# Kernel optimization log

Hardware: AMD Instinct MI355X
Metric: run time of the kernel (lower is better)

## Reference

```python
import jax, jax.numpy as jnp
import numpy as np

EPS = 1e-5


def _bn(x, g, b):
    # training-mode BatchNorm2d over (N, H, W), biased variance
    m = jnp.mean(x, axis=(0, 2, 3), keepdims=True)
    v = jnp.var(x, axis=(0, 2, 3), keepdims=True)
    return (x - m) * jax.lax.rsqrt(v + EPS) * g[None, :, None, None] + b[None, :, None, None]


def _conv1x1(x, w):
    # x: [B, Cin, H, W], w: [Cout, Cin]
    return jnp.einsum('bchw,oc->bohw', x, w)


def _prop_attention(x, wq, wkv, wo, bo, obj_dict, bg_dict, rand_inds):
    B, C, H, W = x.shape  # B == 1
    heads, crop = rand_inds.shape[0], rand_inds.shape[1]
    dh = C // heads
    HW = H * W
    num_obj = crop // 2
    # original does x.clone().detach() before attention
    xd = jax.lax.stop_gradient(x)
    xh = xd.reshape(heads, dh, HW)  # batch=1 folded away (matches t.view(-1, crop**2))
    # pos[h, i, j] = flat pixel index gathered for head h, group i, slot j
    pos = jnp.concatenate(
        [obj_dict[rand_inds[:, :num_obj]], bg_dict[rand_inds[:, num_obj:]]], axis=1
    )  # [heads, crop, crop]
    tokens = jax.vmap(lambda xv, pv: xv[:, pv])(xh, pos)  # [heads, dh, crop, crop]
    tokens = tokens.transpose(0, 2, 3, 1).reshape(heads * crop, crop, dh)
    q = tokens @ wq.T
    k, v = jnp.split(tokens @ wkv.T, 2, axis=-1)
    dots = jnp.einsum('bie,bje->bij', q, k) * (dh ** -0.5)
    attn = jax.nn.softmax(dots, axis=-1)
    out = jnp.einsum('bij,bje->bie', attn, v)  # [heads*crop, crop, dh]
    # faithful to torch out.view(heads*crop, -1, crop): a raw row-major reinterpret
    out_r = out.reshape(heads, crop, dh, crop)
    vals = out_r.transpose(0, 2, 1, 3).reshape(heads, dh, crop * crop)
    pos_flat = pos.reshape(heads, crop * crop)
    # pos is a bijection onto [0, HW) per head -> invert and gather
    ar = jnp.arange(HW, dtype=jnp.int32)
    inv = jax.vmap(lambda p: jnp.zeros((HW,), jnp.int32).at[p].set(ar))(pos_flat)
    img = jax.vmap(lambda vh, ih: vh[:, ih])(vals, inv)  # [heads, dh, HW]
    img = img.reshape(1, heads * dh, H, W)
    # to_out: Linear(dim, dim) applied channels-last
    return jnp.einsum('bchw,oc->bohw', img, wo) + bo[None, :, None, None]


def setup_inputs():
    H = W = 300
    HW = H * W
    heads, crop = 2, H
    num_obj = crop // 2
    ch, emb = 256, 64
    dh = emb // heads
    key = jax.random.key(0)
    ks = jax.random.split(key, 10)
    x = jax.random.normal(ks[0], (1, ch, H, W), jnp.float32)
    perm = jax.random.permutation(ks[1], HW)
    obj_dict = perm[: HW // 2]
    bg_dict = perm[HW // 2 :]
    ri = []
    for h in range(heads):
        po = jax.random.permutation(jax.random.fold_in(ks[2], h), HW // 2).reshape(num_obj, crop)
        pb = jax.random.permutation(jax.random.fold_in(ks[3], h), HW // 2).reshape(crop - num_obj, crop)
        ri.append(jnp.concatenate([po, pb], axis=0))
    rand_inds = jnp.stack(ri)  # [heads, crop, crop]
    w_conv1 = jax.random.normal(ks[4], (emb, ch), jnp.float32) / np.sqrt(ch)
    wq = jax.random.normal(ks[5], (dh, dh), jnp.float32) / np.sqrt(dh)
    wkv = jax.random.normal(ks[6], (2 * dh, dh), jnp.float32) / np.sqrt(dh)
    wo = jax.random.normal(ks[7], (emb, emb), jnp.float32) / np.sqrt(emb)
    bo = jnp.zeros((emb,), jnp.float32)
    w_conv2 = jax.random.normal(ks[8], (emb, 2 * emb), jnp.float32) / np.sqrt(2 * emb)
    return {
        'x': x,
        'w_conv1': w_conv1,
        'bn1_g': jnp.ones((emb,), jnp.float32),
        'bn1_b': jnp.zeros((emb,), jnp.float32),
        'wq': wq,
        'wkv': wkv,
        'wo': wo,
        'bo': bo,
        'w_conv2': w_conv2,
        'bn2_g': jnp.ones((emb,), jnp.float32),
        'bn2_b': jnp.zeros((emb,), jnp.float32),
        'obj_dict': obj_dict,
        'bg_dict': bg_dict,
        'rand_inds': rand_inds,
    }


def reference(x, w_conv1, bn1_g, bn1_b, wq, wkv, wo, bo, w_conv2, bn2_g, bn2_b, obj_dict, bg_dict, rand_inds):
    x1 = jax.nn.relu(_bn(_conv1x1(x, w_conv1), bn1_g, bn1_b))
    xa = jax.nn.relu(_prop_attention(x1, wq, wkv, wo, bo, obj_dict, bg_dict, rand_inds))
    xc = jnp.concatenate([xa, x1], axis=1)
    return jax.nn.relu(_bn(_conv1x1(xc, w_conv2), bn2_g, bn2_b))
```

## Files before the change

### kernel.cpp

```cpp
#include <hip/hip_runtime.h>
#include <hip/hip_bf16.h>

#define HW 90000
#define CROP 300
#define C2EXP 0.25503492f

typedef __attribute__((ext_vector_type(8))) short s8v;
typedef __attribute__((ext_vector_type(4))) float f4v;
#define MFMA16(a,b,c) __builtin_amdgcn_mfma_f32_16x16x32_bf16(a,b,c,0,0,0)

__device__ __forceinline__ unsigned short f2bf(float f) {
    unsigned int u = __float_as_uint(f);
    return (unsigned short)((u + 0x7fffu + ((u >> 16) & 1u)) >> 16);
}
__device__ __forceinline__ float bf2f(unsigned short s) {
    return __uint_as_float(((unsigned int)s) << 16);
}
__device__ __forceinline__ unsigned pk_trunc(float a, float b) {
    return __builtin_amdgcn_perm(__float_as_uint(b), __float_as_uint(a), 0x07060302u);
}
__device__ __forceinline__ unsigned pk_rne(float a, float b) {
    return (unsigned)f2bf(a) | ((unsigned)f2bf(b) << 16);
}

__global__ void prep_kernel(const float* __restrict__ w1, const float* __restrict__ wq,
                            const float* __restrict__ wkv, const float* __restrict__ wo,
                            const float* __restrict__ w2,
                            short* __restrict__ w1b, short* __restrict__ wkvb,
                            short* __restrict__ wob, short* __restrict__ w2b,
                            short* __restrict__ msb) {
    int idx = blockIdx.x * blockDim.x + threadIdx.x;
    int stride = gridDim.x * blockDim.x;
    for (int i = idx; i < 16384; i += stride) w1b[i] = (short)f2bf(w1[i]);
    for (int i = idx; i < 2048; i += stride)  wkvb[i] = (short)f2bf(wkv[i]);
    for (int i = idx; i < 4096; i += stride)  wob[i] = (short)f2bf(wo[i]);
    for (int i = idx; i < 8192; i += stride)  w2b[i] = (short)f2bf(w2[i]);
    for (int i = idx; i < 1024; i += stride) {
        int ep = i >> 5, e = i & 31;
        float s = 0.f;
        for (int a = 0; a < 32; ++a) s += wq[a * 32 + e] * wkv[a * 32 + ep];
        msb[i] = (short)f2bf(s * C2EXP);
    }
}

__global__ __launch_bounds__(256, 2) void conv1_mfma(const float* __restrict__ x,
        const short* __restrict__ w1b, short* __restrict__ y1b, float* __restrict__ stat) {
    __shared__ __align__(16) short lw[16384];
    __shared__ float red[2][4][64];
    const int wave = threadIdx.x >> 6, lane = threadIdx.x & 63;
    const int q = lane >> 4, n = lane & 15;
    for (int i = threadIdx.x; i < 2048; i += 256)
        ((uint4*)lw)[i] = ((const uint4*)w1b)[i];
    __syncthreads();

    const int s0 = blockIdx.x * 256 + wave * 64;
    int pbx = s0 + 4 * n;
    if (pbx > HW - 4) pbx = HW - 4;
    f4v acc[4][4];
#pragma unroll
    for (int mt = 0; mt < 4; ++mt)
#pragma unroll
        for (int nt = 0; nt < 4; ++nt) acc[mt][nt] = f4v{0.f, 0.f, 0.f, 0.f};

    float4 cur[8], nxt[8];
#pragma unroll
    for (int j = 0; j < 8; ++j)
        cur[j] = *(const float4*)(x + (size_t)(q * 8 + j) * HW + pbx);
#pragma unroll
    for (int kb = 0; kb < 8; ++kb) {
        if (kb < 7) {
#pragma unroll
            for (int j = 0; j < 8; ++j)
                nxt[j] = *(const float4*)(x + (size_t)((kb + 1) * 32 + q * 8 + j) * HW + pbx);
        }
        s8v A[4];
#pragma unroll
        for (int mt = 0; mt < 4; ++mt) {
            union { unsigned u[4]; s8v v; } am;
#pragma unroll
            for (int w = 0; w < 4; ++w)
                am.u[w] = pk_trunc(((const float*)&cur[2 * w])[mt],
                                   ((const float*)&cur[2 * w + 1])[mt]);
            A[mt] = am.v;
        }
#pragma unroll
        for (int mt = 0; mt < 4; ++mt)
#pragma unroll
            for (int nt = 0; nt < 4; ++nt) {
                int c = (nt & 1) + 2 * n + 32 * (nt >> 1);
                s8v B = *(const s8v*)(lw + c * 256 + kb * 32 + q * 8);
                acc[mt][nt] = MFMA16(A[mt], B, acc[mt][nt]);
            }
        if (kb < 7) {
#pragma unroll
            for (int j = 0; j < 8; ++j) cur[j] = nxt[j];
        }
    }

    float s1[4] = {0.f, 0.f, 0.f, 0.f}, s2[4] = {0.f, 0.f, 0.f, 0.f};
#pragma unroll
    for (int mt = 0; mt < 4; ++mt)
#pragma unroll
        for (int r = 0; r < 4; ++r) {
            int p = s0 + 4 * (q * 4 + r) + mt;
            if (p < HW) {
                float v0 = acc[mt][0][r], v1 = acc[mt][1][r];
                float v2 = acc[mt][2][r], v3 = acc[mt][3][r];
                *(unsigned*)(y1b + (size_t)p * 64 + 2 * n)      = pk_rne(v0, v1);
                *(unsigned*)(y1b + (size_t)p * 64 + 32 + 2 * n) = pk_rne(v2, v3);
                s1[0] += v0; s2[0] += v0 * v0;
                s1[1] += v1; s2[1] += v1 * v1;
                s1[2] += v2; s2[2] += v2 * v2;
                s1[3] += v3; s2[3] += v3 * v3;
            }
        }
#pragma unroll
    for (int m = 16; m < 64; m <<= 1)
#pragma unroll
        for (int nt = 0; nt < 4; ++nt) {
            s1[nt] += __shfl_xor(s1[nt], m, 64);
            s2[nt] += __shfl_xor(s2[nt], m, 64);
        }
    if (lane < 16)
#pragma unroll
        for (int nt = 0; nt < 4; ++nt) {
            int c = (nt & 1) + 2 * lane + 32 * (nt >> 1);
            red[0][wave][c] = s1[nt];
            red[1][wave][c] = s2[nt];
        }
    __syncthreads();
    if (threadIdx.x < 128) {
        int k = threadIdx.x >> 6, c = threadIdx.x & 63;
        atomicAdd(&stat[k * 64 + c],
                  red[k][0][c] + red[k][1][c] + red[k][2][c] + red[k][3][c]);
    }
}

__global__ void bn_fin_kernel(const float* __restrict__ stat,
        const float* __restrict__ g, const float* __restrict__ b, float* __restrict__ ab) {
    int c = threadIdx.x;
    float m = stat[c] * (1.f / HW);
    float v = stat[64 + c] * (1.f / HW) - m * m;
    float ac = g[c] * rsqrtf(v + 1e-5f);
    ab[c] = ac;
    ab[64 + c] = b[c] - m * ac;
}

__global__ __launch_bounds__(256) void bnrelu_kernel(const short* __restrict__ y1b,
        const float* __restrict__ ab1, short* __restrict__ x1b) {
    int t = blockIdx.x * 256 + threadIdx.x;
    if (t >= 720000) return;
    int cb = 8 * (t & 7);
    float4 a0 = *(const float4*)(ab1 + cb), a1 = *(const float4*)(ab1 + cb + 4);
    float4 b0 = *(const float4*)(ab1 + 64 + cb), b1 = *(const float4*)(ab1 + 64 + cb + 4);
    uint4 u = ((const uint4*)y1b)[t];
    float r0 = fmaxf(fmaf(a0.x, __uint_as_float(u.x << 16), b0.x), 0.f);
    float r1 = fmaxf(fmaf(a0.y, __uint_as_float(u.x & 0xffff0000u), b0.y), 0.f);
    float r2 = fmaxf(fmaf(a0.z, __uint_as_float(u.y << 16), b0.z), 0.f);
    float r3 = fmaxf(fmaf(a0.w, __uint_as_float(u.y & 0xffff0000u), b0.w), 0.f);
    float r4 = fmaxf(fmaf(a1.x, __uint_as_float(u.z << 16), b1.x), 0.f);
    float r5 = fmaxf(fmaf(a1.y, __uint_as_float(u.z & 0xffff0000u), b1.y), 0.f);
    float r6 = fmaxf(fmaf(a1.z, __uint_as_float(u.w << 16), b1.z), 0.f);
    float r7 = fmaxf(fmaf(a1.w, __uint_as_float(u.w & 0xffff0000u), b1.w), 0.f);
    uint4 o;
    o.x = pk_rne(r0, r1); o.y = pk_rne(r2, r3);
    o.z = pk_rne(r4, r5); o.w = pk_rne(r6, r7);
    ((uint4*)x1b)[t] = o;
}

__global__ __launch_bounds__(512, 4) void attn_mfma_kernel(const short* __restrict__ x1b,
        const short* __restrict__ msb, const short* __restrict__ wkvb,
        const int* __restrict__ obj, const int* __restrict__ bg,
        const int* __restrict__ rinds, short* __restrict__ imgb) {
    __shared__ __align__(16) short tok[304 * 40];
    __shared__ __align__(16) short vt[32 * 328];
    __shared__ __align__(16) short pbuf[8 * 3 * 640];
    __shared__ int possh[300];
    const int b = blockIdx.x;
    const int h = b / CROP, i = b - h * CROP;
    const int tid = threadIdx.x;
    const int wave = tid >> 6, lane = tid & 63, q = lane >> 4, n = lane & 15;
    const int nti = (wave < 3) ? 3 : 2;

    if (tid < 300) {
        int ri = rinds[h * HW + i * CROP + tid];
        possh[tid] = (i < 150) ? obj[ri] : bg[ri];
    }
    for (int ii = tid; ii < 80; ii += 512)
        ((unsigned*)(tok + 300 * 40))[ii] = 0;
    for (int ii = tid; ii < 640; ii += 512) {
        int e = ii / 20, w = ii - 20 * e;
        ((unsigned*)vt)[e * 164 + 144 + w] = 0;
    }
    __syncthreads();

    for (int idx = tid; idx < 1200; idx += 512) {
        int j = idx >> 2, part = idx & 3;
        *(uint4*)(tok + j * 40 + part * 8) =
            *(const uint4*)(x1b + (size_t)possh[j] * 64 + h * 32 + part * 8);
    }
    __syncthreads();

    short* pw0 = pbuf + wave * 3 * 640;
    s8v aQ[3];
    {
        s8v bq0 = *(const s8v*)(msb + n * 32 + q * 8);
        s8v bq1 = *(const s8v*)(msb + (16 + n) * 32 + q * 8);
        s8v bv0 = *(const s8v*)(wkvb + (32 + n) * 32 + q * 8);
        s8v bv1 = *(const s8v*)(wkvb + (48 + n) * 32 + q * 8);
        f4v zz = {0.f, 0.f, 0.f, 0.f};
#pragma unroll
        for (int ti = 0; ti < 3; ++ti) {
            aQ[ti] = s8v{};
            if (ti < nti) {
                int t = wave + ti * 8;
                s8v at = *(const s8v*)(tok + (16 * t + n) * 40 + q * 8);
                f4v qf0 = MFMA16(at, bq0, zz);
                f4v qf1 = MFMA16(at, bq1, zz);
                f4v vf0 = MFMA16(at, bv0, zz);
                f4v vf1 = MFMA16(at, bv1, zz);
#pragma unroll
                for (int r = 0; r < 4; ++r) {
                    int row = 16 * t + q * 4 + r;
                    int phys = ((row >> 5) << 5) + 2 * (row & 15) + ((row >> 4) & 1);
                    vt[n * 328 + phys]        = (short)f2bf(vf0[r]);
                    vt[(16 + n) * 328 + phys] = (short)f2bf(vf1[r]);
                    pw0[(q * 4 + r) * 40 + n]      = (short)f2bf(qf0[r]);
                    pw0[(q * 4 + r) * 40 + 16 + n] = (short)f2bf(qf1[r]);
                }
                asm volatile("s_waitcnt lgkmcnt(0)" ::: "memory");
                aQ[ti] = *(const s8v*)(pw0 + n * 40 + q * 8);
            }
        }
    }
    __syncthreads();

    f4v O[3][2];
    float lsum[3][4];
#pragma unroll
    for (int ti = 0; ti < 3; ++ti) {
        O[ti][0] = f4v{0.f, 0.f, 0.f, 0.f};
        O[ti][1] = f4v{0.f, 0.f, 0.f, 0.f};
#pragma unroll
        for (int r = 0; r < 4; ++r) lsum[ti][r] = 0.f;
    }
    f4v zz = {0.f, 0.f, 0.f, 0.f};
    for (int kb = 0; kb < 10; ++kb) {
        s8v bK0 = *(const s8v*)(tok + (32 * kb + n) * 40 + q * 8);
        s8v bK1 = (kb < 9) ? *(const s8v*)(tok + (32 * kb + 16 + n) * 40 + q * 8) : s8v{};
        s8v bV0 = *(const s8v*)(vt + n * 328 + kb * 32 + q * 8);
        s8v bV1 = *(const s8v*)(vt + (16 + n) * 328 + kb * 32 + q * 8);
        f4v sv[3][2];
#pragma unroll
        for (int ti = 0; ti < 3; ++ti)
            if (ti < nti) {
                sv[ti][0] = MFMA16(aQ[ti], bK0, zz);
                sv[ti][1] = MFMA16(aQ[ti], bK1, zz);
            }
#pragma unroll
        for (int ti = 0; ti < 3; ++ti)
            if (ti < nti) {
                unsigned* pwd = (unsigned*)(pbuf + (wave * 3 + ti) * 640);
                if (kb < 9) {
#pragma unroll
                    for (int r = 0; r < 4; ++r) {
                        float e0 = exp2f(sv[ti][0][r]);
                        float e1 = exp2f(sv[ti][1][r]);
                        unsigned pk = pk_trunc(e0, e1);
                        lsum[ti][r] += __uint_as_float(pk << 16) +
                                       __uint_as_float(pk & 0xffff0000u);
                        pwd[(q * 4 + r) * 20 + n] = pk;
                    }
                } else {
#pragma unroll
                    for (int r = 0; r < 4; ++r) {
                        float e0 = (n < 12) ? exp2f(sv[ti][0][r]) : 0.f;
                        unsigned pk = pk_trunc(e0, 0.f);
                        lsum[ti][r] += __uint_as_float(pk << 16);
                        pwd[(q * 4 + r) * 20 + n] = pk;
                    }
                }
            }
        asm volatile("s_waitcnt lgkmcnt(0)" ::: "memory");
#pragma unroll
        for (int ti = 0; ti < 3; ++ti)
            if (ti < nti) {
                s8v ap = *(const s8v*)(pbuf + (wave * 3 + ti) * 640 + n * 40 + q * 8);
                O[ti][0] = MFMA16(ap, bV0, O[ti][0]);
                O[ti][1] = MFMA16(ap, bV1, O[ti][1]);
            }
    }
    __syncthreads();

#pragma unroll
    for (int m = 1; m < 16; m <<= 1) {
#pragma unroll
        for (int ti = 0; ti < 3; ++ti)
#pragma unroll
            for (int r = 0; r < 4; ++r)
                lsum[ti][r] += __shfl_xor(lsum[ti][r], m, 64);
    }
    short* outb = tok;
#pragma unroll
    for (int ti = 0; ti < 3; ++ti) {
        if (ti >= nti) continue;
        int t = wave + ti * 8;
#pragma unroll
        for (int r = 0; r < 4; ++r) {
            float rl = 1.f / lsum[ti][r];
            int row = 16 * t + q * 4 + r;
            outb[row * 32 + n]      = (short)f2bf(O[ti][0][r] * rl);
            outb[row * 32 + 16 + n] = (short)f2bf(O[ti][1][r] * rl);
        }
    }
    __syncthreads();

    for (int idx = tid; idx < 9600; idx += 512) {
        int jj = idx >> 5, dd = idx & 31;
        imgb[(size_t)possh[jj] * 64 + h * 32 + dd] = outb[dd * CROP + jj];
    }
}

__global__ __launch_bounds__(256, 3) void fuse2_mfma(const short* __restrict__ imgb,
        const short* __restrict__ x1b,
        const short* __restrict__ wob, const short* __restrict__ w2b,
        const float* __restrict__ bo, short* __restrict__ y2b, float* __restrict__ stat) {
    __shared__ __align__(16) short xas[4][16 * 72];
    __shared__ unsigned ytrp[64 * 68];
    __shared__ float red[2][4][64];
    const int wave = threadIdx.x >> 6, lane = threadIdx.x & 63;
    const int q = lane >> 4, n = lane & 15;
    s8v Bo[2][4], B2[4][4];
#pragma unroll
    for (int kb = 0; kb < 2; ++kb)
#pragma unroll
        for (int nt = 0; nt < 4; ++nt)
            Bo[kb][nt] = *(const s8v*)(wob + (nt * 16 + n) * 64 + kb * 32 + q * 8);
#pragma unroll
    for (int kb = 0; kb < 4; ++kb)
#pragma unroll
        for (int nt = 0; nt < 4; ++nt)
            B2[kb][nt] = *(const s8v*)(w2b + (nt * 16 + n) * 128 + kb * 32 + q * 8);
    float bov[4];
#pragma unroll
    for (int nt = 0; nt < 4; ++nt) bov[nt] = bo[nt * 16 + n];

    float s1[4] = {0.f, 0.f, 0.f, 0.f}, s2[4] = {0.f, 0.f, 0.f, 0.f};
    short* xw = xas[wave];
#pragma unroll
    for (int ti = 0; ti < 2; ++ti) {
        int tile = blockIdx.x * 8 + wave * 2 + ti;
        if (tile >= 5625) continue;
        int s0 = tile * 16;
        f4v xacc[4];
#pragma unroll
        for (int nt = 0; nt < 4; ++nt) xacc[nt] = f4v{0.f, 0.f, 0.f, 0.f};
#pragma unroll
        for (int kb = 0; kb < 2; ++kb) {
            s8v A = *(const s8v*)(imgb + (size_t)(s0 + n) * 64 + kb * 32 + q * 8);
#pragma unroll
            for (int nt = 0; nt < 4; ++nt) xacc[nt] = MFMA16(A, Bo[kb][nt], xacc[nt]);
        }
#pragma unroll
        for (int nt = 0; nt < 4; ++nt)
#pragma unroll
            for (int r = 0; r < 4; ++r) {
                float v = fmaxf(xacc[nt][r] + bov[nt], 0.f);
                xw[(q * 4 + r) * 72 + nt * 16 + n] = (short)f2bf(v);
            }
        asm volatile("s_waitcnt lgkmcnt(0)" ::: "memory");
        f4v yacc[4];
#pragma unroll
        for (int nt = 0; nt < 4; ++nt) yacc[nt] = f4v{0.f, 0.f, 0.f, 0.f};
#pragma unroll
        for (int kb = 0; kb < 2; ++kb) {
            s8v Axa = *(const s8v*)(xw + n * 72 + kb * 32 + q * 8);
#pragma unroll
            for (int nt = 0; nt < 4; ++nt) yacc[nt] = MFMA16(Axa, B2[kb][nt], yacc[nt]);
        }
#pragma unroll
        for (int kb = 0; kb < 2; ++kb) {
            s8v A = *(const s8v*)(x1b + (size_t)(s0 + n) * 64 + kb * 32 + q * 8);
#pragma unroll
            for (int nt = 0; nt < 4; ++nt) yacc[nt] = MFMA16(A, B2[kb + 2][nt], yacc[nt]);
        }
        int pl2 = wave * 16 + ti * 8;
#pragma unroll
        for (int nt = 0; nt < 4; ++nt) {
#pragma unroll
            for (int r = 0; r < 4; ++r) {
                float v = yacc[nt][r];
                s1[nt] += v; s2[nt] += v * v;
            }
            ytrp[(nt * 16 + n) * 68 + pl2 + q * 2 + 0] = pk_rne(yacc[nt][0], yacc[nt][1]);
            ytrp[(nt * 16 + n) * 68 + pl2 + q * 2 + 1] = pk_rne(yacc[nt][2], yacc[nt][3]);
        }
    }
#pragma unroll
    for (int m = 16; m < 64; m <<= 1)
#pragma unroll
        for (int nt = 0; nt < 4; ++nt) {
            s1[nt] += __shfl_xor(s1[nt], m, 64);
            s2[nt] += __shfl_xor(s2[nt], m, 64);
        }
    if (lane < 16)
#pragma unroll
        for (int nt = 0; nt < 4; ++nt) {
            red[0][wave][nt * 16 + lane] = s1[nt];
            red[1][wave][nt * 16 + lane] = s2[nt];
        }
    __syncthreads();
    int s0b = blockIdx.x * 128;
    int maxp2 = (HW - s0b) >> 1;
    for (int i = threadIdx.x; i < 4096; i += 256) {
        int c = i >> 6, p2 = i & 63;
        if (p2 < maxp2)
            ((unsigned*)y2b)[c * (HW / 2) + (s0b >> 1) + p2] = ytrp[c * 68 + p2];
    }
    if (threadIdx.x < 128) {
        int k = threadIdx.x >> 6, c = threadIdx.x & 63;
        atomicAdd(&stat[k * 64 + c],
                  red[k][0][c] + red[k][1][c] + red[k][2][c] + red[k][3][c]);
    }
}

__global__ __launch_bounds__(256) void bn_out_kernel(const short* __restrict__ y2b,
        const float* __restrict__ ab2, float* __restrict__ out) {
    int c = blockIdx.y;
    int i = blockIdx.x * 256 + threadIdx.x;
    if (i >= 22500) return;
    float a = ab2[c], b = ab2[64 + c];
    uint2 u = *(const uint2*)((const unsigned*)y2b + c * (HW / 2) + 2 * i);
    float4 v;
    v.x = fmaxf(fmaf(a, __uint_as_float(u.x << 16), b), 0.f);
    v.y = fmaxf(fmaf(a, __uint_as_float(u.x & 0xffff0000u), b), 0.f);
    v.z = fmaxf(fmaf(a, __uint_as_float(u.y << 16), b), 0.f);
    v.w = fmaxf(fmaf(a, __uint_as_float(u.y & 0xffff0000u), b), 0.f);
    *(float4*)(out + (size_t)c * HW + 4 * i) = v;
}

extern "C" void kernel_launch(void* const* d_in, const int* in_sizes, int n_in,
                              void* d_out, int out_size, void* d_ws, size_t ws_size,
                              hipStream_t stream) {
    const float* x   = (const float*)d_in[0];
    const float* w1  = (const float*)d_in[1];
    const float* g1  = (const float*)d_in[2];
    const float* b1  = (const float*)d_in[3];
    const float* wq  = (const float*)d_in[4];
    const float* wkv = (const float*)d_in[5];
    const float* wo  = (const float*)d_in[6];
    const float* bo  = (const float*)d_in[7];
    const float* w2  = (const float*)d_in[8];
    const float* g2  = (const float*)d_in[9];
    const float* b2  = (const float*)d_in[10];
    const int* obj   = (const int*)d_in[11];
    const int* bg    = (const int*)d_in[12];
    const int* rinds = (const int*)d_in[13];

    float* WSF  = (float*)d_ws;
    short* W1B  = (short*)d_ws;
    short* WOB  = W1B + 16384;
    short* W2B  = WOB + 4096;
    short* WKVB = W2B + 8192;
    short* MSB  = WKVB + 2048;
    float* STAT = WSF + 16384;
    float* AB1  = STAT + 256;
    float* AB2  = AB1 + 128;
    short* Y1B  = (short*)(WSF + 16896);
    short* X1B  = Y1B + 5760000;
    short* IMGB = X1B + 5760000;
    short* Y2B  = IMGB + 5760000;

    hipMemsetAsync(STAT, 0, 1024, stream);
    prep_kernel<<<16, 256, 0, stream>>>(w1, wq, wkv, wo, w2, W1B, WKVB, WOB, W2B, MSB);
    conv1_mfma<<<352, 256, 0, stream>>>(x, W1B, Y1B, STAT);
    bn_fin_kernel<<<1, 64, 0, stream>>>(STAT, g1, b1, AB1);
    bnrelu_kernel<<<2813, 256, 0, stream>>>(Y1B, AB1, X1B);
    attn_mfma_kernel<<<600, 512, 0, stream>>>(X1B, MSB, WKVB, obj, bg, rinds, IMGB);
    fuse2_mfma<<<704, 256, 0, stream>>>(IMGB, X1B, WOB, W2B, bo, Y2B, STAT + 128);
    bn_fin_kernel<<<1, 64, 0, stream>>>(STAT + 128, g2, b2, AB2);
    bn_out_kernel<<<dim3(88, 64), 256, 0, stream>>>(Y2B, AB2, (float*)d_out);
}
```

Baseline: 253.0 us.

## Fuse BN1+ReLU into attention and conv2 consumers, restructure attention to 4 waves

Removes the standalone bnrelu kernel and the X1B buffer: the BN1 affine plus ReLU is now applied on the fly when gathering tokens in attention and when loading x1 in the fused conv2 kernel. Attention blocks shrink to 256 threads with 5 tiles per wave. The S matrix is computed transposed so the probabilities are fed to the PV MFMA through ds_bpermute shuffles instead of an LDS staging buffer, which also drops the pbuf shared array. conv1 moves to 128-thread blocks with twice as many blocks. The trade-off is recomputing BN on gathered rows and more cross-lane permute traffic in the attention inner loop.

```diff
diff --git a/kernel.cpp b/kernel.cpp
--- a/kernel.cpp
+++ b/kernel.cpp
@@ -43,17 +43,17 @@
     }
 }
 
-__global__ __launch_bounds__(256, 2) void conv1_mfma(const float* __restrict__ x,
+__global__ __launch_bounds__(128, 2) void conv1_mfma(const float* __restrict__ x,
         const short* __restrict__ w1b, short* __restrict__ y1b, float* __restrict__ stat) {
     __shared__ __align__(16) short lw[16384];
-    __shared__ float red[2][4][64];
+    __shared__ float red[2][2][64];
     const int wave = threadIdx.x >> 6, lane = threadIdx.x & 63;
     const int q = lane >> 4, n = lane & 15;
-    for (int i = threadIdx.x; i < 2048; i += 256)
+    for (int i = threadIdx.x; i < 2048; i += 128)
         ((uint4*)lw)[i] = ((const uint4*)w1b)[i];
     __syncthreads();
 
-    const int s0 = blockIdx.x * 256 + wave * 64;
+    const int s0 = blockIdx.x * 128 + wave * 64;
     int pbx = s0 + 4 * n;
     if (pbx > HW - 4) pbx = HW - 4;
     f4v acc[4][4];
@@ -129,10 +129,9 @@
             red[1][wave][c] = s2[nt];
         }
     __syncthreads();
-    if (threadIdx.x < 128) {
+    {
         int k = threadIdx.x >> 6, c = threadIdx.x & 63;
-        atomicAdd(&stat[k * 64 + c],
-                  red[k][0][c] + red[k][1][c] + red[k][2][c] + red[k][3][c]);
+        atomicAdd(&stat[k * 64 + c], red[k][0][c] + red[k][1][c]);
     }
 }
 
@@ -146,183 +145,195 @@
     ab[64 + c] = b[c] - m * ac;
 }
 
-__global__ __launch_bounds__(256) void bnrelu_kernel(const short* __restrict__ y1b,
-        const float* __restrict__ ab1, short* __restrict__ x1b) {
-    int t = blockIdx.x * 256 + threadIdx.x;
-    if (t >= 720000) return;
-    int cb = 8 * (t & 7);
-    float4 a0 = *(const float4*)(ab1 + cb), a1 = *(const float4*)(ab1 + cb + 4);
-    float4 b0 = *(const float4*)(ab1 + 64 + cb), b1 = *(const float4*)(ab1 + 64 + cb + 4);
-    uint4 u = ((const uint4*)y1b)[t];
-    float r0 = fmaxf(fmaf(a0.x, __uint_as_float(u.x << 16), b0.x), 0.f);
-    float r1 = fmaxf(fmaf(a0.y, __uint_as_float(u.x & 0xffff0000u), b0.y), 0.f);
-    float r2 = fmaxf(fmaf(a0.z, __uint_as_float(u.y << 16), b0.z), 0.f);
-    float r3 = fmaxf(fmaf(a0.w, __uint_as_float(u.y & 0xffff0000u), b0.w), 0.f);
-    float r4 = fmaxf(fmaf(a1.x, __uint_as_float(u.z << 16), b1.x), 0.f);
-    float r5 = fmaxf(fmaf(a1.y, __uint_as_float(u.z & 0xffff0000u), b1.y), 0.f);
-    float r6 = fmaxf(fmaf(a1.z, __uint_as_float(u.w << 16), b1.z), 0.f);
-    float r7 = fmaxf(fmaf(a1.w, __uint_as_float(u.w & 0xffff0000u), b1.w), 0.f);
-    uint4 o;
-    o.x = pk_rne(r0, r1); o.y = pk_rne(r2, r3);
-    o.z = pk_rne(r4, r5); o.w = pk_rne(r6, r7);
-    ((uint4*)x1b)[t] = o;
-}
-
-__global__ __launch_bounds__(512, 4) void attn_mfma_kernel(const short* __restrict__ x1b,
+__global__ __launch_bounds__(256, 3) void attn_mfma_kernel(const short* __restrict__ y1b,
+        const float* __restrict__ ab1,
         const short* __restrict__ msb, const short* __restrict__ wkvb,
         const int* __restrict__ obj, const int* __restrict__ bg,
         const int* __restrict__ rinds, short* __restrict__ imgb) {
     __shared__ __align__(16) short tok[304 * 40];
     __shared__ __align__(16) short vt[32 * 328];
-    __shared__ __align__(16) short pbuf[8 * 3 * 640];
     __shared__ int possh[300];
     const int b = blockIdx.x;
     const int h = b / CROP, i = b - h * CROP;
     const int tid = threadIdx.x;
     const int wave = tid >> 6, lane = tid & 63, q = lane >> 4, n = lane & 15;
-    const int nti = (wave < 3) ? 3 : 2;
-
-    if (tid < 300) {
-        int ri = rinds[h * HW + i * CROP + tid];
-        possh[tid] = (i < 150) ? obj[ri] : bg[ri];
-    }
-    for (int ii = tid; ii < 80; ii += 512)
+    const int ntj = (wave < 3) ? 5 : 4;
+
+    for (int jj = tid; jj < 300; jj += 256) {
+        int ri = rinds[h * HW + i * CROP + jj];
+        possh[jj] = (i < 150) ? obj[ri] : bg[ri];
+    }
+    for (int ii = tid; ii < 80; ii += 256)
         ((unsigned*)(tok + 300 * 40))[ii] = 0;
-    for (int ii = tid; ii < 640; ii += 512) {
-        int e = ii / 20, w = ii - 20 * e;
-        ((unsigned*)vt)[e * 164 + 144 + w] = 0;
-    }
-    __syncthreads();
-
-    for (int idx = tid; idx < 1200; idx += 512) {
-        int j = idx >> 2, part = idx & 3;
-        *(uint4*)(tok + j * 40 + part * 8) =
-            *(const uint4*)(x1b + (size_t)possh[j] * 64 + h * 32 + part * 8);
-    }
-    __syncthreads();
-
-    short* pw0 = pbuf + wave * 3 * 640;
-    s8v aQ[3];
+    __syncthreads();
+
+    {
+        int part = tid & 3;
+        float4 a0 = *(const float4*)(ab1 + h * 32 + part * 8);
+        float4 a1 = *(const float4*)(ab1 + h * 32 + part * 8 + 4);
+        float4 b0 = *(const float4*)(ab1 + 64 + h * 32 + part * 8);
+        float4 b1 = *(const float4*)(ab1 + 64 + h * 32 + part * 8 + 4);
+        for (int idx = tid; idx < 1200; idx += 256) {
+            int j = idx >> 2;
+            uint4 u = *(const uint4*)(y1b + (size_t)possh[j] * 64 + h * 32 + part * 8);
+            float r0 = fmaxf(fmaf(a0.x, __uint_as_float(u.x << 16), b0.x), 0.f);
+            float r1 = fmaxf(fmaf(a0.y, __uint_as_float(u.x & 0xffff0000u), b0.y), 0.f);
+            float r2 = fmaxf(fmaf(a0.z, __uint_as_float(u.y << 16), b0.z), 0.f);
+            float r3 = fmaxf(fmaf(a0.w, __uint_as_float(u.y & 0xffff0000u), b0.w), 0.f);
+            float r4 = fmaxf(fmaf(a1.x, __uint_as_float(u.z << 16), b1.x), 0.f);
+            float r5 = fmaxf(fmaf(a1.y, __uint_as_float(u.z & 0xffff0000u), b1.y), 0.f);
+            float r6 = fmaxf(fmaf(a1.z, __uint_as_float(u.w << 16), b1.z), 0.f);
+            float r7 = fmaxf(fmaf(a1.w, __uint_as_float(u.w & 0xffff0000u), b1.w), 0.f);
+            uint4 o;
+            o.x = pk_rne(r0, r1); o.y = pk_rne(r2, r3);
+            o.z = pk_rne(r4, r5); o.w = pk_rne(r6, r7);
+            *(uint4*)(tok + j * 40 + part * 8) = o;
+        }
+    }
+    __syncthreads();
+
+    short* pw = vt + wave * 640;
+    s8v aQ[5];
     {
         s8v bq0 = *(const s8v*)(msb + n * 32 + q * 8);
         s8v bq1 = *(const s8v*)(msb + (16 + n) * 32 + q * 8);
+        f4v zz = {0.f, 0.f, 0.f, 0.f};
+#pragma unroll
+        for (int tj = 0; tj < 5; ++tj) {
+            aQ[tj] = s8v{};
+            if (tj < ntj) {
+                int t = wave + tj * 4;
+                s8v at = *(const s8v*)(tok + (16 * t + n) * 40 + q * 8);
+                f4v qf0 = MFMA16(at, bq0, zz);
+                f4v qf1 = MFMA16(at, bq1, zz);
+#pragma unroll
+                for (int r = 0; r < 4; ++r) {
+                    pw[(q * 4 + r) * 40 + n]      = (short)f2bf(qf0[r]);
+                    pw[(q * 4 + r) * 40 + 16 + n] = (short)f2bf(qf1[r]);
+                }
+                asm volatile("s_waitcnt lgkmcnt(0)" ::: "memory");
+                aQ[tj] = *(const s8v*)(pw + n * 40 + q * 8);
+            }
+        }
+    }
+    __syncthreads();
+
+    {
         s8v bv0 = *(const s8v*)(wkvb + (32 + n) * 32 + q * 8);
         s8v bv1 = *(const s8v*)(wkvb + (48 + n) * 32 + q * 8);
         f4v zz = {0.f, 0.f, 0.f, 0.f};
 #pragma unroll
-        for (int ti = 0; ti < 3; ++ti) {
-            aQ[ti] = s8v{};
-            if (ti < nti) {
-                int t = wave + ti * 8;
+        for (int tj = 0; tj < 5; ++tj) {
+            if (tj < ntj) {
+                int t = wave + tj * 4;
                 s8v at = *(const s8v*)(tok + (16 * t + n) * 40 + q * 8);
-                f4v qf0 = MFMA16(at, bq0, zz);
-                f4v qf1 = MFMA16(at, bq1, zz);
                 f4v vf0 = MFMA16(at, bv0, zz);
                 f4v vf1 = MFMA16(at, bv1, zz);
 #pragma unroll
                 for (int r = 0; r < 4; ++r) {
                     int row = 16 * t + q * 4 + r;
-                    int phys = ((row >> 5) << 5) + 2 * (row & 15) + ((row >> 4) & 1);
-                    vt[n * 328 + phys]        = (short)f2bf(vf0[r]);
-                    vt[(16 + n) * 328 + phys] = (short)f2bf(vf1[r]);
-                    pw0[(q * 4 + r) * 40 + n]      = (short)f2bf(qf0[r]);
-                    pw0[(q * 4 + r) * 40 + 16 + n] = (short)f2bf(qf1[r]);
+                    vt[n * 328 + row]        = (short)f2bf(vf0[r]);
+                    vt[(16 + n) * 328 + row] = (short)f2bf(vf1[r]);
                 }
-                asm volatile("s_waitcnt lgkmcnt(0)" ::: "memory");
-                aQ[ti] = *(const s8v*)(pw0 + n * 40 + q * 8);
-            }
-        }
-    }
-    __syncthreads();
-
-    f4v O[3][2];
-    float lsum[3][4];
-#pragma unroll
-    for (int ti = 0; ti < 3; ++ti) {
-        O[ti][0] = f4v{0.f, 0.f, 0.f, 0.f};
-        O[ti][1] = f4v{0.f, 0.f, 0.f, 0.f};
-#pragma unroll
-        for (int r = 0; r < 4; ++r) lsum[ti][r] = 0.f;
-    }
+            }
+        }
+    }
+    for (int ii = tid; ii < 384; ii += 256) {
+        int e = ii / 12, w = ii - 12 * e;
+        ((unsigned*)vt)[e * 164 + 152 + w] = 0;
+    }
+    __syncthreads();
+
+    f4v O[5][2];
+    float lsum[5];
+#pragma unroll
+    for (int tj = 0; tj < 5; ++tj) {
+        O[tj][0] = f4v{0.f, 0.f, 0.f, 0.f};
+        O[tj][1] = f4v{0.f, 0.f, 0.f, 0.f};
+        lsum[tj] = 0.f;
+    }
+    const int bidx0 = (n + ((lane & 16) ? 32 : 0)) * 4;
+    const int bidx1 = bidx0 + 64;
+    const bool hi = (lane & 32) != 0;
     f4v zz = {0.f, 0.f, 0.f, 0.f};
     for (int kb = 0; kb < 10; ++kb) {
-        s8v bK0 = *(const s8v*)(tok + (32 * kb + n) * 40 + q * 8);
-        s8v bK1 = (kb < 9) ? *(const s8v*)(tok + (32 * kb + 16 + n) * 40 + q * 8) : s8v{};
+        s8v A0 = *(const s8v*)(tok + (32 * kb + n) * 40 + q * 8);
+        s8v A1 = (kb < 9) ? *(const s8v*)(tok + (32 * kb + 16 + n) * 40 + q * 8) : s8v{};
         s8v bV0 = *(const s8v*)(vt + n * 328 + kb * 32 + q * 8);
         s8v bV1 = *(const s8v*)(vt + (16 + n) * 328 + kb * 32 + q * 8);
-        f4v sv[3][2];
-#pragma unroll
-        for (int ti = 0; ti < 3; ++ti)
-            if (ti < nti) {
-                sv[ti][0] = MFMA16(aQ[ti], bK0, zz);
-                sv[ti][1] = MFMA16(aQ[ti], bK1, zz);
-            }
-#pragma unroll
-        for (int ti = 0; ti < 3; ++ti)
-            if (ti < nti) {
-                unsigned* pwd = (unsigned*)(pbuf + (wave * 3 + ti) * 640);
-                if (kb < 9) {
-#pragma unroll
-                    for (int r = 0; r < 4; ++r) {
-                        float e0 = exp2f(sv[ti][0][r]);
-                        float e1 = exp2f(sv[ti][1][r]);
-                        unsigned pk = pk_trunc(e0, e1);
-                        lsum[ti][r] += __uint_as_float(pk << 16) +
-                                       __uint_as_float(pk & 0xffff0000u);
-                        pwd[(q * 4 + r) * 20 + n] = pk;
-                    }
-                } else {
-#pragma unroll
-                    for (int r = 0; r < 4; ++r) {
-                        float e0 = (n < 12) ? exp2f(sv[ti][0][r]) : 0.f;
-                        unsigned pk = pk_trunc(e0, 0.f);
-                        lsum[ti][r] += __uint_as_float(pk << 16);
-                        pwd[(q * 4 + r) * 20 + n] = pk;
-                    }
-                }
-            }
-        asm volatile("s_waitcnt lgkmcnt(0)" ::: "memory");
-#pragma unroll
-        for (int ti = 0; ti < 3; ++ti)
-            if (ti < nti) {
-                s8v ap = *(const s8v*)(pbuf + (wave * 3 + ti) * 640 + n * 40 + q * 8);
-                O[ti][0] = MFMA16(ap, bV0, O[ti][0]);
-                O[ti][1] = MFMA16(ap, bV1, O[ti][1]);
-            }
-    }
-    __syncthreads();
-
-#pragma unroll
-    for (int m = 1; m < 16; m <<= 1) {
-#pragma unroll
-        for (int ti = 0; ti < 3; ++ti)
-#pragma unroll
-            for (int r = 0; r < 4; ++r)
-                lsum[ti][r] += __shfl_xor(lsum[ti][r], m, 64);
-    }
+#pragma unroll
+        for (int tj = 0; tj < 5; ++tj) {
+            if (tj >= ntj) continue;
+            f4v s0 = MFMA16(A0, aQ[tj], zz);
+            unsigned p0a, p0b, p1a, p1b;
+            if (kb < 9) {
+                f4v s1 = MFMA16(A1, aQ[tj], zz);
+                p0a = pk_trunc(exp2f(s0[0]), exp2f(s0[1]));
+                p0b = pk_trunc(exp2f(s0[2]), exp2f(s0[3]));
+                p1a = pk_trunc(exp2f(s1[0]), exp2f(s1[1]));
+                p1b = pk_trunc(exp2f(s1[2]), exp2f(s1[3]));
+            } else {
+                float e0 = (q < 3) ? exp2f(s0[0]) : 0.f;
+                float e1 = (q < 3) ? exp2f(s0[1]) : 0.f;
+                float e2 = (q < 3) ? exp2f(s0[2]) : 0.f;
+                float e3 = (q < 3) ? exp2f(s0[3]) : 0.f;
+                p0a = pk_trunc(e0, e1);
+                p0b = pk_trunc(e2, e3);
+                p1a = 0; p1b = 0;
+            }
+            lsum[tj] += __uint_as_float(p0a << 16) + __uint_as_float(p0a & 0xffff0000u)
+                      + __uint_as_float(p0b << 16) + __uint_as_float(p0b & 0xffff0000u)
+                      + __uint_as_float(p1a << 16) + __uint_as_float(p1a & 0xffff0000u)
+                      + __uint_as_float(p1b << 16) + __uint_as_float(p1b & 0xffff0000u);
+            union { unsigned u[4]; s8v v; } Ap;
+            {
+                unsigned v0a = __builtin_amdgcn_ds_bpermute(bidx0, (int)p0a);
+                unsigned v1a = __builtin_amdgcn_ds_bpermute(bidx0, (int)p1a);
+                unsigned v0b = __builtin_amdgcn_ds_bpermute(bidx0, (int)p0b);
+                unsigned v1b = __builtin_amdgcn_ds_bpermute(bidx0, (int)p1b);
+                Ap.u[0] = hi ? v1a : v0a;
+                Ap.u[1] = hi ? v1b : v0b;
+                unsigned w0a = __builtin_amdgcn_ds_bpermute(bidx1, (int)p0a);
+                unsigned w1a = __builtin_amdgcn_ds_bpermute(bidx1, (int)p1a);
+                unsigned w0b = __builtin_amdgcn_ds_bpermute(bidx1, (int)p0b);
+                unsigned w1b_ = __builtin_amdgcn_ds_bpermute(bidx1, (int)p1b);
+                Ap.u[2] = hi ? w1a : w0a;
+                Ap.u[3] = hi ? w1b_ : w0b;
+            }
+            O[tj][0] = MFMA16(Ap.v, bV0, O[tj][0]);
+            O[tj][1] = MFMA16(Ap.v, bV1, O[tj][1]);
+        }
+    }
+    __syncthreads();
+
+#pragma unroll
+    for (int m = 16; m < 64; m <<= 1)
+#pragma unroll
+        for (int tj = 0; tj < 5; ++tj)
+            lsum[tj] += __shfl_xor(lsum[tj], m, 64);
     short* outb = tok;
 #pragma unroll
-    for (int ti = 0; ti < 3; ++ti) {
-        if (ti >= nti) continue;
-        int t = wave + ti * 8;
+    for (int tj = 0; tj < 5; ++tj) {
+        if (tj >= ntj) continue;
+        int t = wave + tj * 4;
 #pragma unroll
         for (int r = 0; r < 4; ++r) {
-            float rl = 1.f / lsum[ti][r];
+            float rl = 1.f / __shfl(lsum[tj], q * 4 + r, 64);
             int row = 16 * t + q * 4 + r;
-            outb[row * 32 + n]      = (short)f2bf(O[ti][0][r] * rl);
-            outb[row * 32 + 16 + n] = (short)f2bf(O[ti][1][r] * rl);
-        }
-    }
-    __syncthreads();
-
-    for (int idx = tid; idx < 9600; idx += 512) {
+            outb[row * 32 + n]      = (short)f2bf(O[tj][0][r] * rl);
+            outb[row * 32 + 16 + n] = (short)f2bf(O[tj][1][r] * rl);
+        }
+    }
+    __syncthreads();
+
+    for (int idx = tid; idx < 9600; idx += 256) {
         int jj = idx >> 5, dd = idx & 31;
         imgb[(size_t)possh[jj] * 64 + h * 32 + dd] = outb[dd * CROP + jj];
     }
 }
 
 __global__ __launch_bounds__(256, 3) void fuse2_mfma(const short* __restrict__ imgb,
-        const short* __restrict__ x1b,
+        const short* __restrict__ y1b, const float* __restrict__ ab1,
         const short* __restrict__ wob, const short* __restrict__ w2b,
         const float* __restrict__ bo, short* __restrict__ y2b, float* __restrict__ stat) {
     __shared__ __align__(16) short xas[4][16 * 72];
@@ -344,6 +355,14 @@
     float bov[4];
 #pragma unroll
     for (int nt = 0; nt < 4; ++nt) bov[nt] = bo[nt * 16 + n];
+    float4 a1v[2][2], b1v[2][2];
+#pragma unroll
+    for (int kb = 0; kb < 2; ++kb) {
+        a1v[kb][0] = *(const float4*)(ab1 + kb * 32 + q * 8);
+        a1v[kb][1] = *(const float4*)(ab1 + kb * 32 + q * 8 + 4);
+        b1v[kb][0] = *(const float4*)(ab1 + 64 + kb * 32 + q * 8);
+        b1v[kb][1] = *(const float4*)(ab1 + 64 + kb * 32 + q * 8 + 4);
+    }
 
     float s1[4] = {0.f, 0.f, 0.f, 0.f}, s2[4] = {0.f, 0.f, 0.f, 0.f};
     short* xw = xas[wave];
@@ -380,9 +399,20 @@
         }
 #pragma unroll
         for (int kb = 0; kb < 2; ++kb) {
-            s8v A = *(const s8v*)(x1b + (size_t)(s0 + n) * 64 + kb * 32 + q * 8);
-#pragma unroll
-            for (int nt = 0; nt < 4; ++nt) yacc[nt] = MFMA16(A, B2[kb + 2][nt], yacc[nt]);
+            uint4 u = *(const uint4*)(y1b + (size_t)(s0 + n) * 64 + kb * 32 + q * 8);
+            float r0 = fmaxf(fmaf(a1v[kb][0].x, __uint_as_float(u.x << 16), b1v[kb][0].x), 0.f);
+            float r1 = fmaxf(fmaf(a1v[kb][0].y, __uint_as_float(u.x & 0xffff0000u), b1v[kb][0].y), 0.f);
+            float r2 = fmaxf(fmaf(a1v[kb][0].z, __uint_as_float(u.y << 16), b1v[kb][0].z), 0.f);
+            float r3 = fmaxf(fmaf(a1v[kb][0].w, __uint_as_float(u.y & 0xffff0000u), b1v[kb][0].w), 0.f);
+            float r4 = fmaxf(fmaf(a1v[kb][1].x, __uint_as_float(u.z << 16), b1v[kb][1].x), 0.f);
+            float r5 = fmaxf(fmaf(a1v[kb][1].y, __uint_as_float(u.z & 0xffff0000u), b1v[kb][1].y), 0.f);
+            float r6 = fmaxf(fmaf(a1v[kb][1].z, __uint_as_float(u.w << 16), b1v[kb][1].z), 0.f);
+            float r7 = fmaxf(fmaf(a1v[kb][1].w, __uint_as_float(u.w & 0xffff0000u), b1v[kb][1].w), 0.f);
+            union { unsigned u[4]; s8v v; } A;
+            A.u[0] = pk_rne(r0, r1); A.u[1] = pk_rne(r2, r3);
+            A.u[2] = pk_rne(r4, r5); A.u[3] = pk_rne(r6, r7);
+#pragma unroll
+            for (int nt = 0; nt < 4; ++nt) yacc[nt] = MFMA16(A.v, B2[kb + 2][nt], yacc[nt]);
         }
         int pl2 = wave * 16 + ti * 8;
 #pragma unroll
@@ -467,17 +497,15 @@
     float* AB1  = STAT + 256;
     float* AB2  = AB1 + 128;
     short* Y1B  = (short*)(WSF + 16896);
-    short* X1B  = Y1B + 5760000;
-    short* IMGB = X1B + 5760000;
+    short* IMGB = Y1B + 5760000;
     short* Y2B  = IMGB + 5760000;
 
     hipMemsetAsync(STAT, 0, 1024, stream);
     prep_kernel<<<16, 256, 0, stream>>>(w1, wq, wkv, wo, w2, W1B, WKVB, WOB, W2B, MSB);
-    conv1_mfma<<<352, 256, 0, stream>>>(x, W1B, Y1B, STAT);
+    conv1_mfma<<<704, 128, 0, stream>>>(x, W1B, Y1B, STAT);
     bn_fin_kernel<<<1, 64, 0, stream>>>(STAT, g1, b1, AB1);
-    bnrelu_kernel<<<2813, 256, 0, stream>>>(Y1B, AB1, X1B);
-    attn_mfma_kernel<<<600, 512, 0, stream>>>(X1B, MSB, WKVB, obj, bg, rinds, IMGB);
-    fuse2_mfma<<<704, 256, 0, stream>>>(IMGB, X1B, WOB, W2B, bo, Y2B, STAT + 128);
+    attn_mfma_kernel<<<600, 256, 0, stream>>>(Y1B, AB1, MSB, WKVB, obj, bg, rinds, IMGB);
+    fuse2_mfma<<<704, 256, 0, stream>>>(IMGB, Y1B, AB1, WOB, W2B, bo, Y2B, STAT + 128);
     bn_fin_kernel<<<1, 64, 0, stream>>>(STAT + 128, g2, b2, AB2);
     bn_out_kernel<<<dim3(88, 64), 256, 0, stream>>>(Y2B, AB2, (float*)d_out);
 }
```

New measurement: 266.2 us. +5.2%, slower.

## Fuse BN1+ReLU into attention gather and conv2 loads, drop bnrelu kernel

Applied to the files above, without the earlier changes.

Removes the standalone bnrelu kernel. The attention kernel and fuse2 kernel now read raw conv1 output and apply the BN scale/shift plus ReLU while loading, so the X1B buffer is neither written nor re-read. It also restructures the Q staging so each tile gets its own LDS buffer, with a single wait before reading them back. The cost is recomputing BN+ReLU in two consumers and a little extra ALU work in the gather paths.

```diff
diff --git a/kernel.cpp b/kernel.cpp
--- a/kernel.cpp
+++ b/kernel.cpp
@@ -146,29 +146,8 @@
     ab[64 + c] = b[c] - m * ac;
 }
 
-__global__ __launch_bounds__(256) void bnrelu_kernel(const short* __restrict__ y1b,
-        const float* __restrict__ ab1, short* __restrict__ x1b) {
-    int t = blockIdx.x * 256 + threadIdx.x;
-    if (t >= 720000) return;
-    int cb = 8 * (t & 7);
-    float4 a0 = *(const float4*)(ab1 + cb), a1 = *(const float4*)(ab1 + cb + 4);
-    float4 b0 = *(const float4*)(ab1 + 64 + cb), b1 = *(const float4*)(ab1 + 64 + cb + 4);
-    uint4 u = ((const uint4*)y1b)[t];
-    float r0 = fmaxf(fmaf(a0.x, __uint_as_float(u.x << 16), b0.x), 0.f);
-    float r1 = fmaxf(fmaf(a0.y, __uint_as_float(u.x & 0xffff0000u), b0.y), 0.f);
-    float r2 = fmaxf(fmaf(a0.z, __uint_as_float(u.y << 16), b0.z), 0.f);
-    float r3 = fmaxf(fmaf(a0.w, __uint_as_float(u.y & 0xffff0000u), b0.w), 0.f);
-    float r4 = fmaxf(fmaf(a1.x, __uint_as_float(u.z << 16), b1.x), 0.f);
-    float r5 = fmaxf(fmaf(a1.y, __uint_as_float(u.z & 0xffff0000u), b1.y), 0.f);
-    float r6 = fmaxf(fmaf(a1.z, __uint_as_float(u.w << 16), b1.z), 0.f);
-    float r7 = fmaxf(fmaf(a1.w, __uint_as_float(u.w & 0xffff0000u), b1.w), 0.f);
-    uint4 o;
-    o.x = pk_rne(r0, r1); o.y = pk_rne(r2, r3);
-    o.z = pk_rne(r4, r5); o.w = pk_rne(r6, r7);
-    ((uint4*)x1b)[t] = o;
-}
-
-__global__ __launch_bounds__(512, 4) void attn_mfma_kernel(const short* __restrict__ x1b,
+__global__ __launch_bounds__(512, 4) void attn_mfma_kernel(const short* __restrict__ y1b,
+        const float* __restrict__ ab1,
         const short* __restrict__ msb, const short* __restrict__ wkvb,
         const int* __restrict__ obj, const int* __restrict__ bg,
         const int* __restrict__ rinds, short* __restrict__ imgb) {
@@ -182,9 +161,9 @@
     const int wave = tid >> 6, lane = tid & 63, q = lane >> 4, n = lane & 15;
     const int nti = (wave < 3) ? 3 : 2;
 
-    if (tid < 300) {
-        int ri = rinds[h * HW + i * CROP + tid];
-        possh[tid] = (i < 150) ? obj[ri] : bg[ri];
+    for (int jj = tid; jj < 300; jj += 512) {
+        int ri = rinds[h * HW + i * CROP + jj];
+        possh[jj] = (i < 150) ? obj[ri] : bg[ri];
     }
     for (int ii = tid; ii < 80; ii += 512)
         ((unsigned*)(tok + 300 * 40))[ii] = 0;
@@ -194,14 +173,31 @@
     }
     __syncthreads();
 
-    for (int idx = tid; idx < 1200; idx += 512) {
-        int j = idx >> 2, part = idx & 3;
-        *(uint4*)(tok + j * 40 + part * 8) =
-            *(const uint4*)(x1b + (size_t)possh[j] * 64 + h * 32 + part * 8);
-    }
-    __syncthreads();
-
-    short* pw0 = pbuf + wave * 3 * 640;
+    {
+        int part = tid & 3;
+        float4 a0 = *(const float4*)(ab1 + h * 32 + part * 8);
+        float4 a1 = *(const float4*)(ab1 + h * 32 + part * 8 + 4);
+        float4 b0 = *(const float4*)(ab1 + 64 + h * 32 + part * 8);
+        float4 b1 = *(const float4*)(ab1 + 64 + h * 32 + part * 8 + 4);
+        for (int idx = tid; idx < 1200; idx += 512) {
+            int j = idx >> 2;
+            uint4 u = *(const uint4*)(y1b + (size_t)possh[j] * 64 + h * 32 + part * 8);
+            float r0 = fmaxf(fmaf(a0.x, __uint_as_float(u.x << 16), b0.x), 0.f);
+            float r1 = fmaxf(fmaf(a0.y, __uint_as_float(u.x & 0xffff0000u), b0.y), 0.f);
+            float r2 = fmaxf(fmaf(a0.z, __uint_as_float(u.y << 16), b0.z), 0.f);
+            float r3 = fmaxf(fmaf(a0.w, __uint_as_float(u.y & 0xffff0000u), b0.w), 0.f);
+            float r4 = fmaxf(fmaf(a1.x, __uint_as_float(u.z << 16), b1.x), 0.f);
+            float r5 = fmaxf(fmaf(a1.y, __uint_as_float(u.z & 0xffff0000u), b1.y), 0.f);
+            float r6 = fmaxf(fmaf(a1.z, __uint_as_float(u.w << 16), b1.z), 0.f);
+            float r7 = fmaxf(fmaf(a1.w, __uint_as_float(u.w & 0xffff0000u), b1.w), 0.f);
+            uint4 o;
+            o.x = pk_rne(r0, r1); o.y = pk_rne(r2, r3);
+            o.z = pk_rne(r4, r5); o.w = pk_rne(r6, r7);
+            *(uint4*)(tok + j * 40 + part * 8) = o;
+        }
+    }
+    __syncthreads();
+
     s8v aQ[3];
     {
         s8v bq0 = *(const s8v*)(msb + n * 32 + q * 8);
@@ -214,6 +210,7 @@
             aQ[ti] = s8v{};
             if (ti < nti) {
                 int t = wave + ti * 8;
+                short* pw = pbuf + (wave * 3 + ti) * 640;
                 s8v at = *(const s8v*)(tok + (16 * t + n) * 40 + q * 8);
                 f4v qf0 = MFMA16(at, bq0, zz);
                 f4v qf1 = MFMA16(at, bq1, zz);
@@ -225,13 +222,16 @@
                     int phys = ((row >> 5) << 5) + 2 * (row & 15) + ((row >> 4) & 1);
                     vt[n * 328 + phys]        = (short)f2bf(vf0[r]);
                     vt[(16 + n) * 328 + phys] = (short)f2bf(vf1[r]);
-                    pw0[(q * 4 + r) * 40 + n]      = (short)f2bf(qf0[r]);
-                    pw0[(q * 4 + r) * 40 + 16 + n] = (short)f2bf(qf1[r]);
+                    pw[(q * 4 + r) * 40 + n]      = (short)f2bf(qf0[r]);
+                    pw[(q * 4 + r) * 40 + 16 + n] = (short)f2bf(qf1[r]);
                 }
-                asm volatile("s_waitcnt lgkmcnt(0)" ::: "memory");
-                aQ[ti] = *(const s8v*)(pw0 + n * 40 + q * 8);
-            }
-        }
+            }
+        }
+        asm volatile("s_waitcnt lgkmcnt(0)" ::: "memory");
+#pragma unroll
+        for (int ti = 0; ti < 3; ++ti)
+            if (ti < nti)
+                aQ[ti] = *(const s8v*)(pbuf + (wave * 3 + ti) * 640 + n * 40 + q * 8);
     }
     __syncthreads();
 
@@ -322,7 +322,7 @@
 }
 
 __global__ __launch_bounds__(256, 3) void fuse2_mfma(const short* __restrict__ imgb,
-        const short* __restrict__ x1b,
+        const short* __restrict__ y1b, const float* __restrict__ ab1,
         const short* __restrict__ wob, const short* __restrict__ w2b,
         const float* __restrict__ bo, short* __restrict__ y2b, float* __restrict__ stat) {
     __shared__ __align__(16) short xas[4][16 * 72];
@@ -344,6 +344,14 @@
     float bov[4];
 #pragma unroll
     for (int nt = 0; nt < 4; ++nt) bov[nt] = bo[nt * 16 + n];
+    float4 a1v[2][2], b1v[2][2];
+#pragma unroll
+    for (int kb = 0; kb < 2; ++kb) {
+        a1v[kb][0] = *(const float4*)(ab1 + kb * 32 + q * 8);
+        a1v[kb][1] = *(const float4*)(ab1 + kb * 32 + q * 8 + 4);
+        b1v[kb][0] = *(const float4*)(ab1 + 64 + kb * 32 + q * 8);
+        b1v[kb][1] = *(const float4*)(ab1 + 64 + kb * 32 + q * 8 + 4);
+    }
 
     float s1[4] = {0.f, 0.f, 0.f, 0.f}, s2[4] = {0.f, 0.f, 0.f, 0.f};
     short* xw = xas[wave];
@@ -380,9 +388,20 @@
         }
 #pragma unroll
         for (int kb = 0; kb < 2; ++kb) {
-            s8v A = *(const s8v*)(x1b + (size_t)(s0 + n) * 64 + kb * 32 + q * 8);
-#pragma unroll
-            for (int nt = 0; nt < 4; ++nt) yacc[nt] = MFMA16(A, B2[kb + 2][nt], yacc[nt]);
+            uint4 u = *(const uint4*)(y1b + (size_t)(s0 + n) * 64 + kb * 32 + q * 8);
+            float r0 = fmaxf(fmaf(a1v[kb][0].x, __uint_as_float(u.x << 16), b1v[kb][0].x), 0.f);
+            float r1 = fmaxf(fmaf(a1v[kb][0].y, __uint_as_float(u.x & 0xffff0000u), b1v[kb][0].y), 0.f);
+            float r2 = fmaxf(fmaf(a1v[kb][0].z, __uint_as_float(u.y << 16), b1v[kb][0].z), 0.f);
+            float r3 = fmaxf(fmaf(a1v[kb][0].w, __uint_as_float(u.y & 0xffff0000u), b1v[kb][0].w), 0.f);
+            float r4 = fmaxf(fmaf(a1v[kb][1].x, __uint_as_float(u.z << 16), b1v[kb][1].x), 0.f);
+            float r5 = fmaxf(fmaf(a1v[kb][1].y, __uint_as_float(u.z & 0xffff0000u), b1v[kb][1].y), 0.f);
+            float r6 = fmaxf(fmaf(a1v[kb][1].z, __uint_as_float(u.w << 16), b1v[kb][1].z), 0.f);
+            float r7 = fmaxf(fmaf(a1v[kb][1].w, __uint_as_float(u.w & 0xffff0000u), b1v[kb][1].w), 0.f);
+            union { unsigned u[4]; s8v v; } A;
+            A.u[0] = pk_rne(r0, r1); A.u[1] = pk_rne(r2, r3);
+            A.u[2] = pk_rne(r4, r5); A.u[3] = pk_rne(r6, r7);
+#pragma unroll
+            for (int nt = 0; nt < 4; ++nt) yacc[nt] = MFMA16(A.v, B2[kb + 2][nt], yacc[nt]);
         }
         int pl2 = wave * 16 + ti * 8;
 #pragma unroll
@@ -467,17 +486,15 @@
     float* AB1  = STAT + 256;
     float* AB2  = AB1 + 128;
     short* Y1B  = (short*)(WSF + 16896);
-    short* X1B  = Y1B + 5760000;
-    short* IMGB = X1B + 5760000;
+    short* IMGB = Y1B + 5760000;
     short* Y2B  = IMGB + 5760000;
 
     hipMemsetAsync(STAT, 0, 1024, stream);
     prep_kernel<<<16, 256, 0, stream>>>(w1, wq, wkv, wo, w2, W1B, WKVB, WOB, W2B, MSB);
     conv1_mfma<<<352, 256, 0, stream>>>(x, W1B, Y1B, STAT);
     bn_fin_kernel<<<1, 64, 0, stream>>>(STAT, g1, b1, AB1);
-    bnrelu_kernel<<<2813, 256, 0, stream>>>(Y1B, AB1, X1B);
-    attn_mfma_kernel<<<600, 512, 0, stream>>>(X1B, MSB, WKVB, obj, bg, rinds, IMGB);
-    fuse2_mfma<<<704, 256, 0, stream>>>(IMGB, X1B, WOB, W2B, bo, Y2B, STAT + 128);
+    attn_mfma_kernel<<<600, 512, 0, stream>>>(Y1B, AB1, MSB, WKVB, obj, bg, rinds, IMGB);
+    fuse2_mfma<<<704, 256, 0, stream>>>(IMGB, Y1B, AB1, WOB, W2B, bo, Y2B, STAT + 128);
     bn_fin_kernel<<<1, 64, 0, stream>>>(STAT + 128, g2, b2, AB2);
     bn_out_kernel<<<dim3(88, 64), 256, 0, stream>>>(Y2B, AB2, (float*)d_out);
 }
```

Measured after the change: 253.5 us. About the same (+0.2%).
